# Performance work log

Measured on AMD Instinct MI355X. Metric: run time of the kernel, lower is better.

## Reference

```python
import jax, jax.numpy as jnp
import numpy as np

B = 2048   # windows per stream
N = 49     # tokens per 7x7 window
C = 192    # dim
H = 6      # heads
D = C // H # head_dim = 32
WH = WW = 7
SCALE = D ** -0.5


def _rel_pos_index():
    coords = np.stack(np.meshgrid(np.arange(WH), np.arange(WW), indexing='ij')).reshape(2, -1)
    rc = (coords[:, :, None] - coords[:, None, :]).transpose(1, 2, 0)  # [N,N,2]
    rc[..., 0] += WH - 1
    rc[..., 1] += WW - 1
    rc[..., 0] *= 2 * WW - 1
    return rc.sum(-1)  # [N,N] ints in [0, 169)

RPI = _rel_pos_index()


def setup_inputs() -> dict:
    key = jax.random.key(0)
    ks = jax.random.split(key, 16)
    w = lambda k, sh: jax.random.normal(k, sh, jnp.float32) * 0.02
    s = lambda v: jnp.asarray(v, jnp.float32)
    return {
        'x_sa': jax.random.normal(ks[0], (2 * B, N, C), jnp.float32),
        'x_ca': jax.random.normal(ks[1], (B, 2 * N, C), jnp.float32),
        'lambda_sa': s(0.1),
        'lambda_ca': s(0.1),
        'sa_enh': s(0.1),
        'ca_enh': s(0.1),
        'W_sa_qkv': w(ks[2], (C, 3 * C)), 'b_sa_qkv': jnp.zeros((3 * C,), jnp.float32),
        'W_sa_ct': w(ks[3], (C, C)), 'W_sa_cr': w(ks[4], (C, C)),
        'W_ca_q': w(ks[5], (C, C)), 'b_ca_q': jnp.zeros((C,), jnp.float32),
        'W_ca_kv': w(ks[6], (C, 2 * C)), 'b_ca_kv': jnp.zeros((2 * C,), jnp.float32),
        'W_ca_ct': w(ks[7], (C, C)), 'W_ca_cr': w(ks[8], (C, C)),
        'rpb_table': w(ks[9], ((2 * WH - 1) * (2 * WW - 1), H)),
        'W_proj_sa': w(ks[10], (C, C)), 'b_proj_sa': jnp.zeros((C,), jnp.float32),
        'W_proj_ca': w(ks[11], (C, C)), 'b_proj_ca': jnp.zeros((C,), jnp.float32),
    }


def _heads(x):  # [B,N,C] -> [B,H,N,D]
    b, n, _ = x.shape
    return x.reshape(b, n, H, D).transpose(0, 2, 1, 3)


def _merge(x):  # [B,H,N,D] -> [B,N,C]
    b = x.shape[0]
    return x.transpose(0, 2, 1, 3).reshape(b, -1, C)


def _diff_attn(qt, kt, vt, qr, kr, vr, bias, lam_param):
    at = jax.nn.softmax(jnp.einsum('bhnd,bhmd->bhnm', qt * SCALE, kt) + bias, axis=-1)
    ar = jax.nn.softmax(jnp.einsum('bhnd,bhmd->bhnm', qr * SCALE, kr) + bias, axis=-1)
    lam = jnp.clip(jax.nn.sigmoid(lam_param), 0.01, 0.99)
    ot = jnp.einsum('bhnm,bhmd->bhnd', at - lam * ar, vt)
    orf = jnp.einsum('bhnm,bhmd->bhnd', ar - lam * at, vr)
    return ot, orf


def _forward(x_sa, x_ca, lambda_sa, lambda_ca, sa_enh, ca_enh,
             W_sa_qkv, b_sa_qkv, W_sa_ct, W_sa_cr,
             W_ca_q, b_ca_q, W_ca_kv, b_ca_kv, W_ca_ct, W_ca_cr,
             rpb_table, W_proj_sa, b_proj_sa, W_proj_ca, b_proj_ca):
    bias = rpb_table[RPI.reshape(-1)].reshape(N, N, H).transpose(2, 0, 1)  # [H,N,N]

    # ---- self-attention path (streams concat on batch) ----
    xt, xr = x_sa[:B], x_sa[B:]
    te = xt + sa_enh * (xr @ W_sa_cr)
    re = xr + sa_enh * (xt @ W_sa_ct)
    qkv_t = (te @ W_sa_qkv + b_sa_qkv).reshape(B, N, 3, H, D).transpose(2, 0, 3, 1, 4)
    qkv_r = (re @ W_sa_qkv + b_sa_qkv).reshape(B, N, 3, H, D).transpose(2, 0, 3, 1, 4)
    ot, orf = _diff_attn(qkv_t[0], qkv_t[1], qkv_t[2], qkv_r[0], qkv_r[1], qkv_r[2], bias, lambda_sa)
    out_sa = jnp.concatenate([_merge(ot) @ W_proj_sa + b_proj_sa,
                              _merge(orf) @ W_proj_sa + b_proj_sa], axis=0)  # [2B,N,C]

    # ---- cross-attention path (streams concat on sequence) ----
    xt, xr = x_ca[:, :N, :], x_ca[:, N:, :]
    te = xt + ca_enh * (xr @ W_ca_cr)
    re = xr + ca_enh * (xt @ W_ca_ct)
    qt = _heads(te @ W_ca_q + b_ca_q)
    qr = _heads(re @ W_ca_q + b_ca_q)
    xcat = jnp.concatenate([te, re], axis=1)  # [B,2N,C]
    kv = (xcat @ W_ca_kv + b_ca_kv).reshape(B, 2 * N, 2, H, D).transpose(2, 0, 3, 1, 4)
    k, v = kv[0], kv[1]  # [B,H,2N,D]
    ot, orf = _diff_attn(qt, k[:, :, :N], v[:, :, :N], qr, k[:, :, N:], v[:, :, N:], bias, lambda_ca)
    out_ca = jnp.concatenate([_merge(ot) @ W_proj_ca + b_proj_ca,
                              _merge(orf) @ W_proj_ca + b_proj_ca], axis=1)  # [B,2N,C]

    return jnp.stack([out_sa, out_ca.reshape(2 * B, N, C)], axis=0)  # [2,2B,N,C]


def reference(x_sa, x_ca, lambda_sa, lambda_ca, sa_enh, ca_enh,
              W_sa_qkv, b_sa_qkv, W_sa_ct, W_sa_cr,
              W_ca_q, b_ca_q, W_ca_kv, b_ca_kv, W_ca_ct, W_ca_cr,
              rpb_table, W_proj_sa, b_proj_sa, W_proj_ca, b_proj_ca):
    return _forward(x_sa, x_ca, lambda_sa, lambda_ca, sa_enh, ca_enh,
                    W_sa_qkv, b_sa_qkv, W_sa_ct, W_sa_cr,
                    W_ca_q, b_ca_q, W_ca_kv, b_ca_kv, W_ca_ct, W_ca_cr,
                    rpb_table, W_proj_sa, b_proj_sa, W_proj_ca, b_proj_ca)
```

## Files before the change

kernel.cpp:

```cpp
#include <hip/hip_runtime.h>
#include <cmath>

static constexpr float SCALE_ = 0.17677669529663687f;

typedef __attribute__((ext_vector_type(8))) _Float16 f16x8;
typedef __attribute__((ext_vector_type(8))) ushort u16x8;
typedef __attribute__((ext_vector_type(4))) float f32x4;

__device__ inline ushort f16u(float f) {
    union { _Float16 h; ushort u; } c;
    c.h = (_Float16)f;
    return c.u;
}

__device__ __forceinline__ void gld16(const ushort* g, ushort* l) {
    __builtin_amdgcn_global_load_lds(
        (const __attribute__((address_space(1))) unsigned int*)g,
        (__attribute__((address_space(3))) unsigned int*)l,
        16, 0, 0);
}

struct SmallmmJobs {
    const float* Wa[6];
    const float* Wb[6];
    const float* sc[6];
    float*       out[6];
    int          NCb[6];
    int          base[7];
};
__global__ __launch_bounds__(256) void smallmm_all(SmallmmJobs J)
{
    int b = blockIdx.x;
    int j = 0;
    #pragma unroll
    for (int k = 1; k < 6; ++k) if (b >= J.base[k]) j = k;
    int idx = (b - J.base[j]) * 256 + threadIdx.x;
    int NCb = J.NCb[j];
    int n4  = NCb >> 2;
    int m   = idx / n4;
    int n0  = (idx - m * n4) << 2;
    if (m >= 192) return;
    const float* Wa = J.Wa[j];
    const float* Wb = J.Wb[j];
    float s = J.sc[j][0];
    float ax = 0.f, ay = 0.f, az = 0.f, aw = 0.f;
    for (int k = 0; k < 192; ++k) {
        float a = Wa[m * 192 + k];
        const float4 bv = *(const float4*)(Wb + (size_t)k * NCb + n0);
        ax += a * bv.x; ay += a * bv.y; az += a * bv.z; aw += a * bv.w;
    }
    float4 r = make_float4(ax * s, ay * s, az * s, aw * s);
    *(float4*)(J.out[j] + (size_t)m * NCb + n0) = r;
}

struct WtJobs {
    const float* W[11];
    ushort*      dh[11];
    int          NC[11];
    int          base[12];
};
__global__ __launch_bounds__(256) void conv_wT_all(WtJobs J)
{
    int b = blockIdx.x;
    int j = 0;
    #pragma unroll
    for (int k = 1; k < 11; ++k) if (b >= J.base[k]) j = k;
    int idx = (b - J.base[j]) * 256 + threadIdx.x;
    int NC = J.NC[j];
    if (idx >= NC * 192) return;
    int n = idx / 192, k = idx - n * 192;
    float f = J.W[j][(long long)k * NC + n];
    long long o = ((long long)(k >> 5) * NC + n) * 32 + (k & 31);
    J.dh[j][o] = f16u(f);
}

__global__ __launch_bounds__(256) void conv_x2(
    const float* __restrict__ src_t, const float* __restrict__ src_r,
    long long src_bs,
    ushort* __restrict__ dh_t, ushort* __restrict__ dh_r, int Mc)
{
    const long long SS = (long long)Mc * 32;
    const long long total8 = (long long)Mc * 24;
    for (long long t = (long long)blockIdx.x * 256 + threadIdx.x; t < 2 * total8;
         t += (long long)gridDim.x * 256) {
        const int second = (t >= total8);
        long long ti = second ? t - total8 : t;
        const float* src = second ? src_r : src_t;
        ushort* dh = second ? dh_r : dh_t;
        int m  = (int)(ti / 24);
        int c8 = (int)(ti - (long long)m * 24) * 8;
        int bb = m / 49, r = m - bb * 49;
        const float* sp = src + (long long)bb * src_bs + r * 192 + c8;
        float4 v0 = *(const float4*)sp;
        float4 v1 = *(const float4*)(sp + 4);
        float f[8] = {v0.x, v0.y, v0.z, v0.w, v1.x, v1.y, v1.z, v1.w};
        u16x8 h8;
        #pragma unroll
        for (int e = 0; e < 8; ++e) h8[e] = f16u(f[e]);
        long long o = (long long)(c8 >> 5) * SS + (long long)m * 32 + (c8 & 31);
        *(u16x8*)(dh + o) = h8;
    }
}

template<int NC, bool DUAL, bool F32OUT>
__global__ __launch_bounds__(256, 4) void gemm_f16(
    const ushort* __restrict__ A1a, const ushort* __restrict__ A2a,
    const ushort* __restrict__ B2a, ushort* __restrict__ outHa,
    float* __restrict__ outFa,
    const ushort* __restrict__ A1b, const ushort* __restrict__ A2b,
    const ushort* __restrict__ B2b, ushort* __restrict__ outHb,
    float* __restrict__ outFb,
    const ushort* __restrict__ B1, const float* __restrict__ bias,
    long long out_bs, int M)
{
    __shared__ __align__(16) ushort AHs[2][2048];
    __shared__ __align__(16) ushort BHs[2][6144];

    constexpr int GX = NC / 192;
    const int nwg = gridDim.x;
    const int orig = blockIdx.x;
    const int q8 = nwg >> 3, r8b = nwg & 7;
    const int xc = orig & 7, ix = orig >> 3;
    const int L = (xc < r8b ? xc * (q8 + 1) : r8b * (q8 + 1) + (xc - r8b) * q8) + ix;
    const int bm = L / (GX * 2);
    const int rem = L - bm * (GX * 2);
    const int bn = rem % GX;
    const int z  = rem / GX;

    const ushort* Ah1 = z ? A1b : A1a;
    const ushort* Ah2 = z ? A2b : A2a;
    const ushort* Bh2 = z ? B2b : B2a;

    const int tid = threadIdx.x;
    const int lane = tid & 63, wv = tid >> 6;
    const int wm = (wv >> 1) * 32;
    const int wn = (wv & 1) * 96;
    const int lr = lane & 15, lg = lane >> 4;
    const long long SS = (long long)M * 32;
    constexpr int NP = DUAL ? 6 : 3;

    const int at_row = tid >> 2;
    const int at_c   = (tid & 3) ^ ((tid >> 3) & 3);
    const long long a_src = (long long)(bm * 64 + at_row) * 32 + at_c * 8;
    int b_src[3];
    #pragma unroll
    for (int k = 0; k < 3; ++k) {
        int t = k * 256 + tid;
        int row = t >> 2, c = (t & 3) ^ ((t >> 3) & 3);
        b_src[k] = (bn * 192 + row) * 32 + c * 8;
    }
    const int wdst = wv * 512;

    int aoff[2], boff[6];
    #pragma unroll
    for (int i = 0; i < 2; ++i) {
        int row = wm + 16 * i + lr;
        aoff[i] = (row * 4 + (lg ^ ((row >> 1) & 3))) * 8;
    }
    #pragma unroll
    for (int j = 0; j < 6; ++j) {
        int row = wn + 16 * j + lr;
        boff[j] = (row * 4 + (lg ^ ((row >> 1) & 3))) * 8;
    }

    f32x4 acc[2][6] = {};

    #pragma unroll
    for (int p = 0; p < NP; ++p) {
        #pragma unroll
        for (int hbf = 0; hbf < 2; ++hbf) {
            const int s = 2 * p + hbf;
            const int k6 = (s < 6) ? s : s - 6;
            const ushort* AHp = (!DUAL || s < 6) ? Ah1 : Ah2;
            const ushort* BHp = (!DUAL || s < 6) ? B1  : Bh2;
            const long long asb = (long long)k6 * SS;
            const int bsb = k6 * (NC * 32);
            gld16(AHp + asb + a_src, AHs[hbf] + wdst);
            #pragma unroll
            for (int k = 0; k < 3; ++k)
                gld16(BHp + bsb + b_src[k], BHs[hbf] + k * 2048 + wdst);
        }
        __syncthreads();

        #pragma unroll
        for (int hbf = 0; hbf < 2; ++hbf) {
            f16x8 ah[2];
            #pragma unroll
            for (int i = 0; i < 2; ++i)
                ah[i] = *(const f16x8*)&AHs[hbf][aoff[i]];
            #pragma unroll
            for (int j = 0; j < 6; ++j) {
                f16x8 bh = *(const f16x8*)&BHs[hbf][boff[j]];
                #pragma unroll
                for (int i = 0; i < 2; ++i)
                    acc[i][j] = __builtin_amdgcn_mfma_f32_16x16x32_f16(ah[i], bh, acc[i][j], 0, 0, 0);
            }
        }
        __syncthreads();
    }

    #pragma unroll
    for (int j = 0; j < 6; ++j) {
        const int c = bn * 192 + wn + 16 * j + lr;
        const float bv = bias ? bias[c] : 0.f;
        #pragma unroll
        for (int i = 0; i < 2; ++i)
            #pragma unroll
            for (int r = 0; r < 4; ++r) {
                int m = bm * 64 + wm + 16 * i + 4 * lg + r;
                if (m < M) {
                    float f = acc[i][j][r] + bv;
                    if constexpr (F32OUT) {
                        float* outF = z ? outFb : outFa;
                        int b2 = m / 49, r2 = m - b2 * 49;
                        outF[(long long)b2 * out_bs + r2 * 192 + c] = f;
                    } else {
                        ushort* outH = z ? outHb : outHa;
                        long long o = (long long)(c >> 5) * SS + (long long)m * 32 + (c & 31);
                        outH[o] = f16u(f);
                    }
                }
            }
    }
}

__global__ __launch_bounds__(256, 4) void attn_f16(
    const ushort* __restrict__ qT, const ushort* __restrict__ kT,
    const ushort* __restrict__ vT,
    const ushort* __restrict__ qR, const ushort* __restrict__ kR,
    const ushort* __restrict__ vR,
    long long SS,
    const float* __restrict__ rpb, const float* __restrict__ lam_ptr,
    ushort* __restrict__ otH, ushort* __restrict__ orH)
{
    __shared__ __align__(16) ushort Pth[64][72];
    __shared__ __align__(16) ushort Vs[2][32][70];
    __shared__ float bias_s[169];

    const int tid = threadIdx.x;
    const int bb = blockIdx.x / 6;
    const int h  = blockIdx.x - bb * 6;
    const int lane = tid & 63;
    const int w  = tid >> 6;
    const int li = lane & 15;
    const int lg = lane >> 4;
    const long long rowbase = (long long)bb * 49 * 32;
    const long long hb = (long long)h * SS + rowbase;

    for (int idx = tid; idx < 169; idx += 256) bias_s[idx] = rpb[idx * 6 + h];

    {
        const ushort* vsrc[2] = {vT + hb, vR + hb};
        for (int c = tid; c < 392; c += 256) {
            int s  = c / 196;
            int r2 = c - s * 196;
            int j  = r2 >> 2;
            int d4 = (r2 & 3) * 8;
            u16x8 v = *(const u16x8*)(vsrc[s] + j * 32 + d4);
            #pragma unroll
            for (int e = 0; e < 8; ++e) Vs[s][d4 + e][j] = v[e];
        }
        for (int c = tid; c < 2 * 32 * 21; c += 256) {
            int s  = c / (32 * 21);
            int r1 = c - s * (32 * 21);
            int d  = r1 / 21;
            int j  = 49 + (r1 - d * 21);
            Vs[s][d][j] = 0;
        }
    }

    float lraw = lam_ptr[0];
    float lam = 1.f / (1.f + __expf(-lraw));
    lam = fminf(fmaxf(lam, 0.01f), 0.99f);

    const int irow = min(w * 16 + li, 48);

    f32x4 st[2][4];
    #pragma unroll
    for (int s = 0; s < 2; ++s) {
        const ushort* qb = (s ? qR : qT) + hb;
        const ushort* kb = (s ? kR : kT) + hb;
        f16x8 qh = *(const f16x8*)(qb + irow * 32 + 8 * lg);
        #pragma unroll
        for (int jt = 0; jt < 4; ++jt) {
            int jr = jt * 16 + li; if (jr > 48) jr = 48;
            f16x8 kh = *(const f16x8*)(kb + jr * 32 + 8 * lg);
            f32x4 c = {};
            c = __builtin_amdgcn_mfma_f32_16x16x32_f16(kh, qh, c, 0, 0, 0);
            st[s][jt] = c;
        }
    }
    __syncthreads();

    const int ri = (irow * 9363) >> 16;
    const int ci = irow - 7 * ri;
    float bias_v[4][4];
    #pragma unroll
    for (int jt = 0; jt < 4; ++jt)
        #pragma unroll
        for (int r = 0; r < 4; ++r) {
            int j = jt * 16 + 4 * lg + r;
            int jc = (j < 49) ? j : 48;
            int rj = (jc * 9363) >> 16;
            int cj = jc - 7 * rj;
            bias_v[jt][r] = bias_s[(ri - rj + 6) * 13 + (ci - cj + 6)];
        }

    float p[2][4][4];
    #pragma unroll
    for (int s = 0; s < 2; ++s) {
        float m = -1e30f;
        #pragma unroll
        for (int jt = 0; jt < 4; ++jt)
            #pragma unroll
            for (int r = 0; r < 4; ++r) {
                int j = jt * 16 + 4 * lg + r;
                float sv = (j < 49) ? (st[s][jt][r] * SCALE_ + bias_v[jt][r]) : -1e30f;
                p[s][jt][r] = sv;
                m = fmaxf(m, sv);
            }
        m = fmaxf(m, __shfl_xor(m, 16));
        m = fmaxf(m, __shfl_xor(m, 32));
        float sum = 0.f;
        #pragma unroll
        for (int jt = 0; jt < 4; ++jt)
            #pragma unroll
            for (int r = 0; r < 4; ++r) {
                float e = __expf(p[s][jt][r] - m);
                p[s][jt][r] = e;
                sum += e;
            }
        sum += __shfl_xor(sum, 16);
        sum += __shfl_xor(sum, 32);
        float inv = 1.f / sum;
        #pragma unroll
        for (int jt = 0; jt < 4; ++jt)
            #pragma unroll
            for (int r = 0; r < 4; ++r)
                p[s][jt][r] *= inv;
    }

    const int prow = w * 16 + li;
    #pragma unroll
    for (int s = 0; s < 2; ++s) {
        #pragma unroll
        for (int jt = 0; jt < 4; ++jt) {
            ushort4 h4;
            #pragma unroll
            for (int r = 0; r < 4; ++r) {
                float at = p[0][jt][r], ar = p[1][jt][r];
                float f = (s == 0) ? (at - lam * ar) : (ar - lam * at);
                ((ushort*)&h4)[r] = f16u(f);
            }
            *(ushort4*)&Pth[prow][jt * 16 + 4 * lg] = h4;
        }

        f32x4 acc[2] = {};
        #pragma unroll
        for (int ks = 0; ks < 2; ++ks) {
            f16x8 pa = *(const f16x8*)&Pth[prow][ks * 32 + 8 * lg];
            #pragma unroll
            for (int dt = 0; dt < 2; ++dt) {
                f16x8 vh = *(const f16x8*)&Vs[s][dt * 16 + li][ks * 32 + 8 * lg];
                acc[dt] = __builtin_amdgcn_mfma_f32_16x16x32_f16(pa, vh, acc[dt], 0, 0, 0);
            }
        }
        ushort* oph = s ? orH : otH;
        #pragma unroll
        for (int dt = 0; dt < 2; ++dt)
            #pragma unroll
            for (int r = 0; r < 4; ++r) {
                int i = w * 16 + 4 * lg + r;
                if (i < 49) {
                    long long o = (long long)h * SS + rowbase + (long long)i * 32 + dt * 16 + li;
                    oph[o] = f16u(acc[dt][r]);
                }
            }
    }
}

extern "C" void kernel_launch(void* const* d_in, const int* in_sizes, int n_in,
                              void* d_out, int out_size, void* d_ws, size_t ws_size,
                              hipStream_t stream)
{
    const float* x_sa      = (const float*)d_in[0];
    const float* x_ca      = (const float*)d_in[1];
    const float* lam_sa    = (const float*)d_in[2];
    const float* lam_ca    = (const float*)d_in[3];
    const float* sa_enh    = (const float*)d_in[4];
    const float* ca_enh    = (const float*)d_in[5];
    const float* W_sa_qkv  = (const float*)d_in[6];
    const float* b_sa_qkv  = (const float*)d_in[7];
    const float* W_sa_ct   = (const float*)d_in[8];
    const float* W_sa_cr   = (const float*)d_in[9];
    const float* W_ca_q    = (const float*)d_in[10];
    const float* b_ca_q    = (const float*)d_in[11];
    const float* W_ca_kv   = (const float*)d_in[12];
    const float* b_ca_kv   = (const float*)d_in[13];
    const float* W_ca_ct   = (const float*)d_in[14];
    const float* W_ca_cr   = (const float*)d_in[15];
    const float* rpb       = (const float*)d_in[16];
    const float* W_proj_sa = (const float*)d_in[17];
    const float* b_proj_sa = (const float*)d_in[18];
    const float* W_proj_ca = (const float*)d_in[19];
    const float* b_proj_ca = (const float*)d_in[20];
    float* out = (float*)d_out;
    float* ws  = (float*)d_ws;

    float* CW0 = ws;
    float* CW1 = CW0 + 110592;
    float* CW2 = CW1 + 110592;
    float* CW3 = CW2 + 36864;
    float* CW4 = CW3 + 36864;
    float* CW5 = CW4 + 73728;

    {
        SmallmmJobs J;
        J.Wa[0]=W_sa_cr; J.Wb[0]=W_sa_qkv; J.sc[0]=sa_enh; J.out[0]=CW0; J.NCb[0]=576;
        J.Wa[1]=W_sa_ct; J.Wb[1]=W_sa_qkv; J.sc[1]=sa_enh; J.out[1]=CW1; J.NCb[1]=576;
        J.Wa[2]=W_ca_cr; J.Wb[2]=W_ca_q;   J.sc[2]=ca_enh; J.out[2]=CW2; J.NCb[2]=192;
        J.Wa[3]=W_ca_ct; J.Wb[3]=W_ca_q;   J.sc[3]=ca_enh; J.out[3]=CW3; J.NCb[3]=192;
        J.Wa[4]=W_ca_cr; J.Wb[4]=W_ca_kv;  J.sc[4]=ca_enh; J.out[4]=CW4; J.NCb[4]=384;
        J.Wa[5]=W_ca_ct; J.Wb[5]=W_ca_kv;  J.sc[5]=ca_enh; J.out[5]=CW5; J.NCb[5]=384;
        int bs[7] = {0,108,216,252,288,360,432};
        for (int i = 0; i < 7; ++i) J.base[i] = bs[i];
        smallmm_all<<<432, 256, 0, stream>>>(J);
    }

    ushort* wb = (ushort*)(ws + 442368);
    ushort* WsaqH = wb;
    ushort* C0H  = WsaqH + 110592;
    ushort* C1H  = C0H + 110592;
    ushort* WcqH = C1H + 110592;
    ushort* C2H  = WcqH + 36864;
    ushort* C3H  = C2H + 36864;
    ushort* WckH = C3H + 36864;
    ushort* C4H  = WckH + 73728;
    ushort* C5H  = C4H + 73728;
    ushort* WpsH = C5H + 73728;
    ushort* WpcH = WpsH + 36864;
    ushort* chunkU = WpcH + 36864;

    {
        WtJobs J;
        const float* Ws[11] = {W_sa_qkv, CW0, CW1, W_ca_q, CW2, CW3,
                               W_ca_kv, CW4, CW5, W_proj_sa, W_proj_ca};
        ushort* Ds[11] = {WsaqH, C0H, C1H, WcqH, C2H, C3H,
                          WckH, C4H, C5H, WpsH, WpcH};
        int NCs[11] = {576,576,576,192,192,192,384,384,384,192,192};
        int bs[12] = {0,432,864,1296,1440,1584,1728,2016,2304,2592,2736,2880};
        for (int i = 0; i < 11; ++i) { J.W[i]=Ws[i]; J.dh[i]=Ds[i]; J.NC[i]=NCs[i]; }
        for (int i = 0; i < 12; ++i) J.base[i] = bs[i];
        conv_wT_all<<<2880, 256, 0, stream>>>(J);
    }

    long long avail = (long long)ws_size - 442368LL * 4 - 737280LL * 2 - 65536;
    int cbmax = (int)(avail / 188160);
    if (cbmax > 1024) cbmax = 1024;
    if (cbmax < 1) cbmax = 1;

    const long long OUT1 = 2LL * 2048 * 49 * 192;
    dim3 blk(256);

    for (int c0 = 0; c0 < 2048; c0 += cbmax) {
        int cb = (c0 + cbmax <= 2048) ? cbmax : (2048 - c0);
        int M = cb * 49;
        long long SS = (long long)M * 32;
        int gy = (M + 63) / 64;
        int cblk = (int)(((long long)M * 48 + 255) / 256);
        if (cblk > 4096) cblk = 4096;

        dim3 g1(6 * gy), g2(2 * gy), g3(4 * gy);

        ushort* XtH = chunkU;
        ushort* XrH = XtH + (long long)cbmax * 9408;
        ushort* QtH = XrH + (long long)cbmax * 9408;
        ushort* QrH = QtH + (long long)cbmax * 28224;
        ushort* OtH = QrH + (long long)cbmax * 28224;
        ushort* OrH = OtH + (long long)cbmax * 9408;

        conv_x2<<<cblk, blk, 0, stream>>>(
            x_sa + (long long)c0 * 9408, x_sa + (2048LL + c0) * 9408, 9408,
            XtH, XrH, M);

        gemm_f16<576, true, false><<<g1, blk, 0, stream>>>(
            XtH, XrH, C0H, QtH, nullptr,
            XrH, XtH, C1H, QrH, nullptr,
            WsaqH, b_sa_qkv, 0, M);

        attn_f16<<<cb * 6, blk, 0, stream>>>(
            QtH, QtH + 6 * SS, QtH + 12 * SS,
            QrH, QrH + 6 * SS, QrH + 12 * SS,
            SS, rpb, lam_sa, OtH, OrH);

        gemm_f16<192, false, true><<<g2, blk, 0, stream>>>(
            OtH, nullptr, nullptr, nullptr, out + (long long)c0 * 9408,
            OrH, nullptr, nullptr, nullptr, out + (2048LL + c0) * 9408,
            WpsH, b_proj_sa, 9408, M);

        ushort* CXtH = chunkU;
        ushort* CXrH = CXtH + (long long)cbmax * 9408;
        ushort* CQtH = CXrH + (long long)cbmax * 9408;
        ushort* CQrH = CQtH + (long long)cbmax * 9408;
        ushort* KtH  = CQrH + (long long)cbmax * 9408;
        ushort* KrH  = KtH + (long long)cbmax * 18816;
        ushort* COtH = KrH + (long long)cbmax * 18816;
        ushort* COrH = COtH + (long long)cbmax * 9408;

        conv_x2<<<cblk, blk, 0, stream>>>(
            x_ca + (long long)c0 * 18816, x_ca + (long long)c0 * 18816 + 9408, 18816,
            CXtH, CXrH, M);

        gemm_f16<192, true, false><<<g2, blk, 0, stream>>>(
            CXtH, CXrH, C2H, CQtH, nullptr,
            CXrH, CXtH, C3H, CQrH, nullptr,
            WcqH, b_ca_q, 0, M);

        gemm_f16<384, true, false><<<g3, blk, 0, stream>>>(
            CXtH, CXrH, C4H, KtH, nullptr,
            CXrH, CXtH, C5H, KrH, nullptr,
            WckH, b_ca_kv, 0, M);

        attn_f16<<<cb * 6, blk, 0, stream>>>(
            CQtH, KtH, KtH + 6 * SS,
            CQrH, KrH, KrH + 6 * SS,
            SS, rpb, lam_ca, COtH, COrH);

        gemm_f16<192, false, true><<<g2, blk, 0, stream>>>(
            COtH, nullptr, nullptr, nullptr, out + OUT1 + (long long)c0 * 18816,
            COrH, nullptr, nullptr, nullptr, out + OUT1 + (long long)c0 * 18816 + 9408,
            WpcH, b_proj_ca, 18816, M);
    }
}
```

Measured before the change: 772.4 us.

## Fuse fp32-to-fp16 input conversion into GEMM A-tile loads

Removes the standalone conv_x2 kernels. The QKV, Q and KV GEMMs now read fp32 activations straight from the inputs, convert them to fp16 in registers and store them into the swizzled LDS A-tile. This cuts two kernel launches per chunk and the fp16 intermediate write and read. Without those intermediate buffers each chunk needs less workspace, so the chunk size grows. The cost is that A is loaded synchronously in fp32, which is twice the bytes, and is re-read once per N-tile block instead of going through async global-to-LDS loads.

```diff
diff --git a/kernel.cpp b/kernel.cpp
--- a/kernel.cpp
+++ b/kernel.cpp
@@ -74,44 +74,16 @@
     J.dh[j][o] = f16u(f);
 }
 
-__global__ __launch_bounds__(256) void conv_x2(
-    const float* __restrict__ src_t, const float* __restrict__ src_r,
-    long long src_bs,
-    ushort* __restrict__ dh_t, ushort* __restrict__ dh_r, int Mc)
-{
-    const long long SS = (long long)Mc * 32;
-    const long long total8 = (long long)Mc * 24;
-    for (long long t = (long long)blockIdx.x * 256 + threadIdx.x; t < 2 * total8;
-         t += (long long)gridDim.x * 256) {
-        const int second = (t >= total8);
-        long long ti = second ? t - total8 : t;
-        const float* src = second ? src_r : src_t;
-        ushort* dh = second ? dh_r : dh_t;
-        int m  = (int)(ti / 24);
-        int c8 = (int)(ti - (long long)m * 24) * 8;
-        int bb = m / 49, r = m - bb * 49;
-        const float* sp = src + (long long)bb * src_bs + r * 192 + c8;
-        float4 v0 = *(const float4*)sp;
-        float4 v1 = *(const float4*)(sp + 4);
-        float f[8] = {v0.x, v0.y, v0.z, v0.w, v1.x, v1.y, v1.z, v1.w};
-        u16x8 h8;
-        #pragma unroll
-        for (int e = 0; e < 8; ++e) h8[e] = f16u(f[e]);
-        long long o = (long long)(c8 >> 5) * SS + (long long)m * 32 + (c8 & 31);
-        *(u16x8*)(dh + o) = h8;
-    }
-}
-
-template<int NC, bool DUAL, bool F32OUT>
+template<int NC, bool DUAL, bool AF32, bool F32OUT>
 __global__ __launch_bounds__(256, 4) void gemm_f16(
-    const ushort* __restrict__ A1a, const ushort* __restrict__ A2a,
+    const void* __restrict__ A1a, const void* __restrict__ A2a,
     const ushort* __restrict__ B2a, ushort* __restrict__ outHa,
     float* __restrict__ outFa,
-    const ushort* __restrict__ A1b, const ushort* __restrict__ A2b,
+    const void* __restrict__ A1b, const void* __restrict__ A2b,
     const ushort* __restrict__ B2b, ushort* __restrict__ outHb,
     float* __restrict__ outFb,
     const ushort* __restrict__ B1, const float* __restrict__ bias,
-    long long out_bs, int M)
+    long long a_bs, long long out_bs, int M)
 {
     __shared__ __align__(16) ushort AHs[2][2048];
     __shared__ __align__(16) ushort BHs[2][6144];
@@ -127,8 +99,8 @@
     const int bn = rem % GX;
     const int z  = rem / GX;
 
-    const ushort* Ah1 = z ? A1b : A1a;
-    const ushort* Ah2 = z ? A2b : A2a;
+    const void* Av1 = z ? A1b : A1a;
+    const void* Av2 = z ? A2b : A2a;
     const ushort* Bh2 = z ? B2b : B2a;
 
     const int tid = threadIdx.x;
@@ -141,7 +113,12 @@
 
     const int at_row = tid >> 2;
     const int at_c   = (tid & 3) ^ ((tid >> 3) & 3);
-    const long long a_src = (long long)(bm * 64 + at_row) * 32 + at_c * 8;
+    int m_l = bm * 64 + at_row;
+    if (m_l >= M) m_l = M - 1;
+    const int abb = m_l / 49, arr = m_l - abb * 49;
+    const long long a_f32 = (long long)abb * a_bs + arr * 192 + at_c * 8;
+    const long long a_u16 = (long long)m_l * 32 + at_c * 8;
+
     int b_src[3];
     #pragma unroll
     for (int k = 0; k < 3; ++k) {
@@ -171,14 +148,25 @@
         for (int hbf = 0; hbf < 2; ++hbf) {
             const int s = 2 * p + hbf;
             const int k6 = (s < 6) ? s : s - 6;
-            const ushort* AHp = (!DUAL || s < 6) ? Ah1 : Ah2;
-            const ushort* BHp = (!DUAL || s < 6) ? B1  : Bh2;
-            const long long asb = (long long)k6 * SS;
+            const ushort* BHp = (!DUAL || s < 6) ? B1 : Bh2;
             const int bsb = k6 * (NC * 32);
-            gld16(AHp + asb + a_src, AHs[hbf] + wdst);
             #pragma unroll
             for (int k = 0; k < 3; ++k)
                 gld16(BHp + bsb + b_src[k], BHs[hbf] + k * 2048 + wdst);
+            if constexpr (AF32) {
+                const float* Af = (const float*)((!DUAL || s < 6) ? Av1 : Av2);
+                const float* sp = Af + a_f32 + k6 * 32;
+                float4 v0 = *(const float4*)sp;
+                float4 v1 = *(const float4*)(sp + 4);
+                float f[8] = {v0.x, v0.y, v0.z, v0.w, v1.x, v1.y, v1.z, v1.w};
+                u16x8 h8;
+                #pragma unroll
+                for (int e = 0; e < 8; ++e) h8[e] = f16u(f[e]);
+                *(u16x8*)&AHs[hbf][tid * 8] = h8;
+            } else {
+                const ushort* AHp = (const ushort*)((!DUAL || s < 6) ? Av1 : Av2);
+                gld16(AHp + (long long)k6 * SS + a_u16, AHs[hbf] + wdst);
+            }
         }
         __syncthreads();
 
@@ -455,7 +443,7 @@
     }
 
     long long avail = (long long)ws_size - 442368LL * 4 - 737280LL * 2 - 65536;
-    int cbmax = (int)(avail / 188160);
+    int cbmax = (int)(avail / 150528);
     if (cbmax > 1024) cbmax = 1024;
     if (cbmax < 1) cbmax = 1;
 
@@ -467,68 +455,59 @@
         int M = cb * 49;
         long long SS = (long long)M * 32;
         int gy = (M + 63) / 64;
-        int cblk = (int)(((long long)M * 48 + 255) / 256);
-        if (cblk > 4096) cblk = 4096;
 
         dim3 g1(6 * gy), g2(2 * gy), g3(4 * gy);
 
-        ushort* XtH = chunkU;
-        ushort* XrH = XtH + (long long)cbmax * 9408;
-        ushort* QtH = XrH + (long long)cbmax * 9408;
+        const float* xt_sa = x_sa + (long long)c0 * 9408;
+        const float* xr_sa = x_sa + (2048LL + c0) * 9408;
+        const float* xt_ca = x_ca + (long long)c0 * 18816;
+        const float* xr_ca = xt_ca + 9408;
+
+        ushort* QtH = chunkU;
         ushort* QrH = QtH + (long long)cbmax * 28224;
         ushort* OtH = QrH + (long long)cbmax * 28224;
         ushort* OrH = OtH + (long long)cbmax * 9408;
 
-        conv_x2<<<cblk, blk, 0, stream>>>(
-            x_sa + (long long)c0 * 9408, x_sa + (2048LL + c0) * 9408, 9408,
-            XtH, XrH, M);
-
-        gemm_f16<576, true, false><<<g1, blk, 0, stream>>>(
-            XtH, XrH, C0H, QtH, nullptr,
-            XrH, XtH, C1H, QrH, nullptr,
-            WsaqH, b_sa_qkv, 0, M);
+        gemm_f16<576, true, true, false><<<g1, blk, 0, stream>>>(
+            xt_sa, xr_sa, C0H, QtH, nullptr,
+            xr_sa, xt_sa, C1H, QrH, nullptr,
+            WsaqH, b_sa_qkv, 9408, 0, M);
 
         attn_f16<<<cb * 6, blk, 0, stream>>>(
             QtH, QtH + 6 * SS, QtH + 12 * SS,
             QrH, QrH + 6 * SS, QrH + 12 * SS,
             SS, rpb, lam_sa, OtH, OrH);
 
-        gemm_f16<192, false, true><<<g2, blk, 0, stream>>>(
+        gemm_f16<192, false, false, true><<<g2, blk, 0, stream>>>(
             OtH, nullptr, nullptr, nullptr, out + (long long)c0 * 9408,
             OrH, nullptr, nullptr, nullptr, out + (2048LL + c0) * 9408,
-            WpsH, b_proj_sa, 9408, M);
-
-        ushort* CXtH = chunkU;
-        ushort* CXrH = CXtH + (long long)cbmax * 9408;
-        ushort* CQtH = CXrH + (long long)cbmax * 9408;
+            WpsH, b_proj_sa, 0, 9408, M);
+
+        ushort* CQtH = chunkU;
         ushort* CQrH = CQtH + (long long)cbmax * 9408;
         ushort* KtH  = CQrH + (long long)cbmax * 9408;
         ushort* KrH  = KtH + (long long)cbmax * 18816;
         ushort* COtH = KrH + (long long)cbmax * 18816;
         ushort* COrH = COtH + (long long)cbmax * 9408;
 
-        conv_x2<<<cblk, blk, 0, stream>>>(
-            x_ca + (long long)c0 * 18816, x_ca + (long long)c0 * 18816 + 9408, 18816,
-            CXtH, CXrH, M);
-
-        gemm_f16<192, true, false><<<g2, blk, 0, stream>>>(
-            CXtH, CXrH, C2H, CQtH, nullptr,
-            CXrH, CXtH, C3H, CQrH, nullptr,
-            WcqH, b_ca_q, 0, M);
-
-        gemm_f16<384, true, false><<<g3, blk, 0, stream>>>(
-            CXtH, CXrH, C4H, KtH, nullptr,
-            CXrH, CXtH, C5H, KrH, nullptr,
-            WckH, b_ca_kv, 0, M);
+        gemm_f16<192, true, true, false><<<g2, blk, 0, stream>>>(
+            xt_ca, xr_ca, C2H, CQtH, nullptr,
+            xr_ca, xt_ca, C3H, CQrH, nullptr,
+            WcqH, b_ca_q, 18816, 0, M);
+
+        gemm_f16<384, true, true, false><<<g3, blk, 0, stream>>>(
+            xt_ca, xr_ca, C4H, KtH, nullptr,
+            xr_ca, xt_ca, C5H, KrH, nullptr,
+            WckH, b_ca_kv, 18816, 0, M);
 
         attn_f16<<<cb * 6, blk, 0, stream>>>(
             CQtH, KtH, KtH + 6 * SS,
             CQrH, KrH, KrH + 6 * SS,
             SS, rpb, lam_ca, COtH, COrH);
 
-        gemm_f16<192, false, true><<<g2, blk, 0, stream>>>(
+        gemm_f16<192, false, false, true><<<g2, blk, 0, stream>>>(
             COtH, nullptr, nullptr, nullptr, out + OUT1 + (long long)c0 * 18816,
             COrH, nullptr, nullptr, nullptr, out + OUT1 + (long long)c0 * 18816 + 9408,
-            WpcH, b_proj_ca, 18816, M);
-    }
-}
+            WpcH, b_proj_ca, 0, 18816, M);
+    }
+}
```

After: 799.8 us. +3.6%, slower.
